# Optimization experiments

Hardware: AMD Instinct MI355X
Metric: run time of the kernel (lower is better)

The kernel has to match this reference:

```python
import jax, jax.numpy as jnp
import numpy as np

B, N, D = 8, 4096, 512

def setup_inputs() -> dict:
    key = jax.random.key(0)
    k1, k2, k3 = jax.random.split(key, 3)
    x = jax.random.normal(k1, (B, N, D), dtype=jnp.float32)
    rotation = jax.random.normal(k2, (D, D), dtype=jnp.float32)
    entangle = jax.random.normal(k3, (D, D), dtype=jnp.float32)
    return {"x": x, "rotation": rotation, "entangle": entangle}

def reference(x, rotation, entangle):
    # query/key projections; note: no V projection, V = x
    query = jnp.einsum("bnd,de->bne", x, rotation)
    key = jnp.einsum("bnd,de->bne", x, entangle)
    scale = 1.0 / jnp.sqrt(jnp.asarray(x.shape[-1], dtype=x.dtype))
    scores = jax.nn.softmax(jnp.einsum("bqd,bkd->bqk", query, key) * scale, axis=-1)
    return jnp.einsum("bqk,bkd->bqd", scores, x)
```

## Files before the change

### kernel.cpp

```cpp
#include <hip/hip_runtime.h>

#define BATCH 8
#define SEQ   4096
#define DIM   512

typedef __attribute__((ext_vector_type(8))) short bf16x8;
typedef __attribute__((ext_vector_type(4))) float f32x4;

__device__ __forceinline__ unsigned short f2bf(float f) {
  unsigned int u = __float_as_uint(f);
  unsigned int r = (u + 0x7fffu + ((u >> 16) & 1u)) >> 16;
  return (unsigned short)r;
}
__device__ __forceinline__ float bf2f(unsigned short s) {
  return __uint_as_float(((unsigned int)s) << 16);
}

__global__ __launch_bounds__(256) void wt_split_kernel(
    const float* __restrict__ rot, const float* __restrict__ ent,
    unsigned short* __restrict__ wrh, unsigned short* __restrict__ wrl,
    unsigned short* __restrict__ weh, unsigned short* __restrict__ wel) {
  const float scale = 0.04419417382415922f;
  int g = blockIdx.x * 256 + threadIdx.x;
  for (int idx = g; idx < 512 * 512; idx += 128 * 256) {
    int d = idx >> 9, e = idx & 511;
    size_t o = (size_t)e * 512 + d;
    float v = rot[idx] * scale;
    unsigned short h = f2bf(v);
    wrh[o] = h; wrl[o] = f2bf(v - bf2f(h));
    float v2 = ent[idx];
    unsigned short h2 = f2bf(v2);
    weh[o] = h2; wel[o] = f2bf(v2 - bf2f(h2));
  }
}

__global__ __launch_bounds__(256) void xt_split_kernel(
    const float* __restrict__ X, unsigned short* __restrict__ Th) {
  __shared__ float T[64][65];
  const int b = blockIdx.z, n0 = blockIdx.x * 64, d0 = blockIdx.y * 64;
  const int tid = threadIdx.x;
  for (int idx = tid; idx < 4096; idx += 256) {
    int r = idx >> 6, c = idx & 63;
    T[r][c] = X[((size_t)(b * SEQ + n0 + r)) * DIM + d0 + c];
  }
  __syncthreads();
  for (int idx = tid; idx < 4096; idx += 256) {
    int r = idx >> 6, c = idx & 63;
    size_t o = ((size_t)(b * DIM + d0 + r)) * SEQ + n0 + c;
    Th[o] = f2bf(T[c][r]);
  }
}

__global__ __launch_bounds__(256, 2) void proj_both(
    const float* __restrict__ X,
    const unsigned short* __restrict__ wrh, const unsigned short* __restrict__ wrl,
    const unsigned short* __restrict__ weh, const unsigned short* __restrict__ wel,
    unsigned short* __restrict__ qh, unsigned short* __restrict__ ql,
    unsigned short* __restrict__ kh, unsigned short* __restrict__ kl) {
  const int tid = threadIdx.x;
  const int w = tid >> 6, lane = tid & 63, l15 = lane & 15, quad = lane >> 4;
  const int rowBase = blockIdx.y * 64 + (w & 1) * 32;
  const int colBase = blockIdx.x * 64 + (w >> 1) * 32;
  f32x4 qa[2][2] = {}, ka[2][2] = {};
  const float* xp[2];
  const unsigned short *rh[2], *rl[2], *eh[2], *el[2];
  xp[0] = X + (size_t)(rowBase + l15) * DIM + quad * 8;
  xp[1] = X + (size_t)(rowBase + 16 + l15) * DIM + quad * 8;
#pragma unroll
  for (int ni = 0; ni < 2; ++ni) {
    size_t o = (size_t)(colBase + ni * 16 + l15) * DIM + quad * 8;
    rh[ni] = wrh + o; rl[ni] = wrl + o; eh[ni] = weh + o; el[ni] = wel + o;
  }
  for (int d0 = 0; d0 < DIM; d0 += 32) {
    bf16x8 ah[2], al[2];
#pragma unroll
    for (int mi = 0; mi < 2; ++mi) {
      const float* p = xp[mi] + d0;
#pragma unroll
      for (int e = 0; e < 8; ++e) {
        float v = p[e];
        unsigned short h = f2bf(v);
        ah[mi][e] = (short)h;
        al[mi][e] = (short)f2bf(v - bf2f(h));
      }
    }
#pragma unroll
    for (int ni = 0; ni < 2; ++ni) {
      bf16x8 bh = *(const bf16x8*)(rh[ni] + d0);
      bf16x8 bl = *(const bf16x8*)(rl[ni] + d0);
      bf16x8 ch = *(const bf16x8*)(eh[ni] + d0);
      bf16x8 cl = *(const bf16x8*)(el[ni] + d0);
#pragma unroll
      for (int mi = 0; mi < 2; ++mi) {
        qa[mi][ni] = __builtin_amdgcn_mfma_f32_16x16x32_bf16(ah[mi], bh, qa[mi][ni], 0, 0, 0);
        qa[mi][ni] = __builtin_amdgcn_mfma_f32_16x16x32_bf16(ah[mi], bl, qa[mi][ni], 0, 0, 0);
        qa[mi][ni] = __builtin_amdgcn_mfma_f32_16x16x32_bf16(al[mi], bh, qa[mi][ni], 0, 0, 0);
        ka[mi][ni] = __builtin_amdgcn_mfma_f32_16x16x32_bf16(ah[mi], ch, ka[mi][ni], 0, 0, 0);
        ka[mi][ni] = __builtin_amdgcn_mfma_f32_16x16x32_bf16(ah[mi], cl, ka[mi][ni], 0, 0, 0);
        ka[mi][ni] = __builtin_amdgcn_mfma_f32_16x16x32_bf16(al[mi], ch, ka[mi][ni], 0, 0, 0);
      }
    }
  }
#pragma unroll
  for (int mi = 0; mi < 2; ++mi)
#pragma unroll
    for (int ni = 0; ni < 2; ++ni)
#pragma unroll
      for (int r = 0; r < 4; ++r) {
        int row = rowBase + mi * 16 + quad * 4 + r;
        int col = colBase + ni * 16 + l15;
        size_t o = (size_t)row * DIM + col;
        float v = qa[mi][ni][r];
        unsigned short h = f2bf(v);
        qh[o] = h; ql[o] = f2bf(v - bf2f(h));
        float v2 = ka[mi][ni][r];
        unsigned short h2 = f2bf(v2);
        kh[o] = h2; kl[o] = f2bf(v2 - bf2f(h2));
      }
}

__global__ __launch_bounds__(256, 2) void attn_mfma(
    const unsigned short* __restrict__ Qh, const unsigned short* __restrict__ Ql,
    const unsigned short* __restrict__ Kh, const unsigned short* __restrict__ Kl,
    const unsigned short* __restrict__ Xth, float* __restrict__ out,
    float* __restrict__ Opart, float* __restrict__ Mp, float* __restrict__ Lp) {
  __shared__ short stage[2][4][2048];
  __shared__ unsigned short PsH[64][72];
  __shared__ float red1[64][2], red2[64][2];
  __shared__ float m_s[64], l_s[64], al_s[64];

  const int tid = threadIdx.x;
  const int w = tid >> 6, lane = tid & 63, l15 = lane & 15, quad = lane >> 4;
  const int b = blockIdx.y, q0 = blockIdx.x * 64;
  const int qsp = (w & 1) * 2, ksp = (w >> 1) * 2;
  const int dbase = w * 128;
  const int ktiles = (SEQ / 64) / gridDim.z;
  const int kbase = blockIdx.z * ktiles * 64;

  if (tid < 64) { m_s[tid] = -3.0e38f; l_s[tid] = 0.0f; }
  __syncthreads();

  f32x4 Of[4][8] = {};

  const int sr = lane >> 2, scm = lane & 3;
  const unsigned short* qsrc = ((w & 1) ? Ql : Qh) + (size_t)(b * SEQ + q0) * DIM;
  const unsigned short* ksrcb = ((w & 1) ? Kl : Kh) + (size_t)b * SEQ * DIM;
  const bool isQ = (w < 2);

  for (int t = 0; t < ktiles; ++t) {
    const int k0 = kbase + t * 64;
    const unsigned short* base = isQ ? qsrc : (ksrcb + (size_t)k0 * DIM);

    {
      bf16x8 g[4];
#pragma unroll
      for (int i = 0; i < 4; ++i) {
        int r = i * 16 + sr, clog = scm ^ (r & 3);
        g[i] = *(const bf16x8*)(base + (size_t)r * DIM + clog * 8);
      }
#pragma unroll
      for (int i = 0; i < 4; ++i) {
        int r = i * 16 + sr;
        *(bf16x8*)&stage[0][w][r * 32 + scm * 8] = g[i];
      }
    }
    __syncthreads();

    f32x4 sa[2][2] = {};
    for (int c = 0; c < 16; ++c) {
      const int bsel = c & 1;
      bf16x8 g[4];
      if (c < 15) {
        const int d0 = (c + 1) * 32;
#pragma unroll
        for (int i = 0; i < 4; ++i) {
          int r = i * 16 + sr, clog = scm ^ (r & 3);
          g[i] = *(const bf16x8*)(base + (size_t)r * DIM + d0 + clog * 8);
        }
      }
      const int cq = (quad ^ (l15 & 3)) * 8;
      bf16x8 a0h = *(const bf16x8*)&stage[bsel][0][((qsp + 0) * 16 + l15) * 32 + cq];
      bf16x8 a0l = *(const bf16x8*)&stage[bsel][1][((qsp + 0) * 16 + l15) * 32 + cq];
      bf16x8 a1h = *(const bf16x8*)&stage[bsel][0][((qsp + 1) * 16 + l15) * 32 + cq];
      bf16x8 a1l = *(const bf16x8*)&stage[bsel][1][((qsp + 1) * 16 + l15) * 32 + cq];
      bf16x8 b0h = *(const bf16x8*)&stage[bsel][2][((ksp + 0) * 16 + l15) * 32 + cq];
      bf16x8 b0l = *(const bf16x8*)&stage[bsel][3][((ksp + 0) * 16 + l15) * 32 + cq];
      bf16x8 b1h = *(const bf16x8*)&stage[bsel][2][((ksp + 1) * 16 + l15) * 32 + cq];
      bf16x8 b1l = *(const bf16x8*)&stage[bsel][3][((ksp + 1) * 16 + l15) * 32 + cq];
      sa[0][0] = __builtin_amdgcn_mfma_f32_16x16x32_bf16(a0h, b0h, sa[0][0], 0, 0, 0);
      sa[0][0] = __builtin_amdgcn_mfma_f32_16x16x32_bf16(a0h, b0l, sa[0][0], 0, 0, 0);
      sa[0][0] = __builtin_amdgcn_mfma_f32_16x16x32_bf16(a0l, b0h, sa[0][0], 0, 0, 0);
      sa[0][1] = __builtin_amdgcn_mfma_f32_16x16x32_bf16(a0h, b1h, sa[0][1], 0, 0, 0);
      sa[0][1] = __builtin_amdgcn_mfma_f32_16x16x32_bf16(a0h, b1l, sa[0][1], 0, 0, 0);
      sa[0][1] = __builtin_amdgcn_mfma_f32_16x16x32_bf16(a0l, b1h, sa[0][1], 0, 0, 0);
      sa[1][0] = __builtin_amdgcn_mfma_f32_16x16x32_bf16(a1h, b0h, sa[1][0], 0, 0, 0);
      sa[1][0] = __builtin_amdgcn_mfma_f32_16x16x32_bf16(a1h, b0l, sa[1][0], 0, 0, 0);
      sa[1][0] = __builtin_amdgcn_mfma_f32_16x16x32_bf16(a1l, b0h, sa[1][0], 0, 0, 0);
      sa[1][1] = __builtin_amdgcn_mfma_f32_16x16x32_bf16(a1h, b1h, sa[1][1], 0, 0, 0);
      sa[1][1] = __builtin_amdgcn_mfma_f32_16x16x32_bf16(a1h, b1l, sa[1][1], 0, 0, 0);
      sa[1][1] = __builtin_amdgcn_mfma_f32_16x16x32_bf16(a1l, b1h, sa[1][1], 0, 0, 0);
      if (c < 15) {
#pragma unroll
        for (int i = 0; i < 4; ++i) {
          int r = i * 16 + sr;
          *(bf16x8*)&stage[1 - bsel][w][r * 32 + scm * 8] = g[i];
        }
      }
      __syncthreads();
    }

    float pm[2][4];
#pragma unroll
    for (int qi = 0; qi < 2; ++qi)
#pragma unroll
      for (int r = 0; r < 4; ++r) {
        float v = fmaxf(sa[qi][0][r], sa[qi][1][r]);
#pragma unroll
        for (int off = 1; off < 16; off <<= 1)
          v = fmaxf(v, __shfl_xor(v, off, 64));
        pm[qi][r] = v;
      }
    if (l15 == 0) {
#pragma unroll
      for (int qi = 0; qi < 2; ++qi)
#pragma unroll
        for (int r = 0; r < 4; ++r)
          red1[(qsp + qi) * 16 + quad * 4 + r][w >> 1] = pm[qi][r];
    }
    __syncthreads();
    if (tid < 64) {
      float mo = m_s[tid];
      float mn = fmaxf(mo, fmaxf(red1[tid][0], red1[tid][1]));
      m_s[tid] = mn;
      al_s[tid] = __expf(mo - mn);
    }
    __syncthreads();

#pragma unroll
    for (int qi = 0; qi < 2; ++qi)
#pragma unroll
      for (int r = 0; r < 4; ++r) {
        const int row = (qsp + qi) * 16 + quad * 4 + r;
        const float m = m_s[row];
        float p0 = __expf(sa[qi][0][r] - m);
        float p1 = __expf(sa[qi][1][r] - m);
        PsH[row][ksp * 16 + l15] = f2bf(p0);
        PsH[row][ksp * 16 + 16 + l15] = f2bf(p1);
        float v = p0 + p1;
#pragma unroll
        for (int off = 1; off < 16; off <<= 1)
          v += __shfl_xor(v, off, 64);
        if (l15 == 0) red2[row][w >> 1] = v;
      }
    __syncthreads();
    if (tid < 64) l_s[tid] = l_s[tid] * al_s[tid] + red2[tid][0] + red2[tid][1];

    float alv[4][4];
#pragma unroll
    for (int qt = 0; qt < 4; ++qt)
#pragma unroll
      for (int r = 0; r < 4; ++r)
        alv[qt][r] = al_s[qt * 16 + quad * 4 + r];
#pragma unroll
    for (int qt = 0; qt < 4; ++qt)
#pragma unroll
      for (int nt = 0; nt < 8; ++nt)
#pragma unroll
        for (int r = 0; r < 4; ++r)
          Of[qt][nt][r] *= alv[qt][r];
#pragma unroll
    for (int ks = 0; ks < 2; ++ks) {
      bf16x8 Ph[4];
#pragma unroll
      for (int qt = 0; qt < 4; ++qt)
        Ph[qt] = *(const bf16x8*)&PsH[qt * 16 + l15][ks * 32 + quad * 8];
      bf16x8 xf[8];
#pragma unroll
      for (int nt = 0; nt < 8; ++nt) {
        const size_t xo =
            ((size_t)(b * DIM + dbase + nt * 16 + l15)) * SEQ + k0 + ks * 32 + quad * 8;
        xf[nt] = *(const bf16x8*)(Xth + xo);
      }
#pragma unroll
      for (int nt = 0; nt < 8; ++nt)
#pragma unroll
        for (int qt = 0; qt < 4; ++qt)
          Of[qt][nt] = __builtin_amdgcn_mfma_f32_16x16x32_bf16(Ph[qt], xf[nt], Of[qt][nt], 0, 0, 0);
    }
    __syncthreads();
  }

  if (gridDim.z == 1) {
    float inv[4][4];
#pragma unroll
    for (int qt = 0; qt < 4; ++qt)
#pragma unroll
      for (int r = 0; r < 4; ++r)
        inv[qt][r] = 1.0f / l_s[qt * 16 + quad * 4 + r];
#pragma unroll
    for (int qt = 0; qt < 4; ++qt)
#pragma unroll
      for (int r = 0; r < 4; ++r) {
        const size_t ro = ((size_t)(b * SEQ + q0 + qt * 16 + quad * 4 + r)) * DIM + dbase;
#pragma unroll
        for (int nt = 0; nt < 8; ++nt)
          out[ro + nt * 16 + l15] = Of[qt][nt][r] * inv[qt][r];
      }
  } else {
    const size_t NE = (size_t)BATCH * SEQ * DIM;
    float* Ob = Opart + (size_t)blockIdx.z * NE;
#pragma unroll
    for (int qt = 0; qt < 4; ++qt)
#pragma unroll
      for (int r = 0; r < 4; ++r) {
        const size_t ro = ((size_t)(b * SEQ + q0 + qt * 16 + quad * 4 + r)) * DIM + dbase;
#pragma unroll
        for (int nt = 0; nt < 8; ++nt)
          Ob[ro + nt * 16 + l15] = Of[qt][nt][r];
      }
    if (tid < 64) {
      size_t ri = (size_t)blockIdx.z * (BATCH * SEQ) + (size_t)b * SEQ + q0 + tid;
      Mp[ri] = m_s[tid];
      Lp[ri] = l_s[tid];
    }
  }
}

__global__ __launch_bounds__(256) void merge_kernel(
    const float* __restrict__ Op, const float* __restrict__ Mp,
    const float* __restrict__ Lp, float* __restrict__ out) {
  const size_t NE = (size_t)BATCH * SEQ * DIM;
  const int NR = BATCH * SEQ;
  size_t i4 = (size_t)blockIdx.x * 256 + threadIdx.x;
  size_t e = i4 * 4;
  int row = (int)(e >> 9);
  float m0 = Mp[row], m1 = Mp[NR + row];
  float l0 = Lp[row], l1 = Lp[NR + row];
  float m = fmaxf(m0, m1);
  float a0 = __expf(m0 - m), a1 = __expf(m1 - m);
  float inv = 1.0f / (a0 * l0 + a1 * l1);
  float4 o0 = *(const float4*)(Op + e);
  float4 o1 = *(const float4*)(Op + NE + e);
  float4 r;
  r.x = (a0 * o0.x + a1 * o1.x) * inv;
  r.y = (a0 * o0.y + a1 * o1.y) * inv;
  r.z = (a0 * o0.z + a1 * o1.z) * inv;
  r.w = (a0 * o0.w + a1 * o1.w) * inv;
  *(float4*)(out + e) = r;
}

extern "C" void kernel_launch(void* const* d_in, const int* in_sizes, int n_in,
                              void* d_out, int out_size, void* d_ws,
                              size_t ws_size, hipStream_t stream) {
  const float* x   = (const float*)d_in[0];
  const float* rot = (const float*)d_in[1];
  const float* ent = (const float*)d_in[2];
  float* out = (float*)d_out;

  const size_t NE = (size_t)BATCH * SEQ * DIM;
  unsigned short* qh  = (unsigned short*)d_ws;
  unsigned short* ql  = qh + NE;
  unsigned short* kh  = ql + NE;
  unsigned short* kl  = kh + NE;
  unsigned short* xth = kl + NE;
  unsigned short* wrh = xth + NE;
  unsigned short* wrl = wrh + 262144;
  unsigned short* weh = wrl + 262144;
  unsigned short* wel = weh + 262144;
  float* Opart = (float*)(wel + 262144);
  float* Mp    = Opart + 2 * NE;
  float* Lp    = Mp + 2 * (BATCH * SEQ);

  const size_t need2 =
      (5 * NE + 4 * 262144) * sizeof(unsigned short) +
      (2 * NE + 4 * (size_t)(BATCH * SEQ)) * sizeof(float);
  const int splits = (ws_size >= need2) ? 2 : 1;

  wt_split_kernel<<<128, 256, 0, stream>>>(rot, ent, wrh, wrl, weh, wel);
  xt_split_kernel<<<dim3(SEQ / 64, DIM / 64, BATCH), 256, 0, stream>>>(x, xth);
  proj_both<<<dim3(DIM / 64, BATCH * SEQ / 64), 256, 0, stream>>>(
      x, wrh, wrl, weh, wel, qh, ql, kh, kl);

  attn_mfma<<<dim3(SEQ / 64, BATCH, splits), 256, 0, stream>>>(
      qh, ql, kh, kl, xth, out, Opart, Mp, Lp);
  if (splits == 2) {
    merge_kernel<<<(unsigned)(NE / 1024), 256, 0, stream>>>(Opart, Mp, Lp, out);
  }
}
```

Baseline: 1.575 ms.

## Restructure attention: register-resident Q, 128-key tiles, direct-to-LDS K loads, presplit X

The attention kernel now keeps each wave's Q fragments (hi/lo bf16) in registers and processes 128 keys per iteration. K tiles stream into LDS through global_load_lds, and the row max and sum are reduced per wave in registers instead of through shared-memory reductions with extra barriers. X is split into bf16 hi/lo once in the transpose kernel, so the projection no longer converts it per tile. Grid ordering is changed, partial output goes straight to out for split 0, and occupancy is raised to 4 blocks. The cost is heavy register pressure (32 Q fragments plus 32 accumulators), which may cause spills at the higher occupancy bound.

```diff
diff --git a/kernel.cpp b/kernel.cpp
--- a/kernel.cpp
+++ b/kernel.cpp
@@ -14,6 +14,12 @@
 }
 __device__ __forceinline__ float bf2f(unsigned short s) {
   return __uint_as_float(((unsigned int)s) << 16);
+}
+
+__device__ __forceinline__ void gload_lds16(const void* g, void* l) {
+  __builtin_amdgcn_global_load_lds(
+      (const __attribute__((address_space(1))) unsigned int*)g,
+      (__attribute__((address_space(3))) unsigned int*)l, 16, 0, 0);
 }
 
 __global__ __launch_bounds__(256) void wt_split_kernel(
@@ -35,13 +41,19 @@
 }
 
 __global__ __launch_bounds__(256) void xt_split_kernel(
-    const float* __restrict__ X, unsigned short* __restrict__ Th) {
+    const float* __restrict__ X, unsigned short* __restrict__ Th,
+    unsigned short* __restrict__ Xh, unsigned short* __restrict__ Xl) {
   __shared__ float T[64][65];
   const int b = blockIdx.z, n0 = blockIdx.x * 64, d0 = blockIdx.y * 64;
   const int tid = threadIdx.x;
   for (int idx = tid; idx < 4096; idx += 256) {
     int r = idx >> 6, c = idx & 63;
-    T[r][c] = X[((size_t)(b * SEQ + n0 + r)) * DIM + d0 + c];
+    size_t gi = ((size_t)(b * SEQ + n0 + r)) * DIM + d0 + c;
+    float v = X[gi];
+    T[r][c] = v;
+    unsigned short h = f2bf(v);
+    Xh[gi] = h;
+    Xl[gi] = f2bf(v - bf2f(h));
   }
   __syncthreads();
   for (int idx = tid; idx < 4096; idx += 256) {
@@ -52,20 +64,23 @@
 }
 
 __global__ __launch_bounds__(256, 2) void proj_both(
-    const float* __restrict__ X,
+    const unsigned short* __restrict__ Xh, const unsigned short* __restrict__ Xl,
     const unsigned short* __restrict__ wrh, const unsigned short* __restrict__ wrl,
     const unsigned short* __restrict__ weh, const unsigned short* __restrict__ wel,
     unsigned short* __restrict__ qh, unsigned short* __restrict__ ql,
     unsigned short* __restrict__ kh, unsigned short* __restrict__ kl) {
   const int tid = threadIdx.x;
   const int w = tid >> 6, lane = tid & 63, l15 = lane & 15, quad = lane >> 4;
-  const int rowBase = blockIdx.y * 64 + (w & 1) * 32;
-  const int colBase = blockIdx.x * 64 + (w >> 1) * 32;
+  const int rowBase = blockIdx.x * 64 + (w & 1) * 32;
+  const int colBase = blockIdx.y * 64 + (w >> 1) * 32;
   f32x4 qa[2][2] = {}, ka[2][2] = {};
-  const float* xp[2];
+  const unsigned short *xph[2], *xpl[2];
   const unsigned short *rh[2], *rl[2], *eh[2], *el[2];
-  xp[0] = X + (size_t)(rowBase + l15) * DIM + quad * 8;
-  xp[1] = X + (size_t)(rowBase + 16 + l15) * DIM + quad * 8;
+#pragma unroll
+  for (int mi = 0; mi < 2; ++mi) {
+    size_t o = (size_t)(rowBase + mi * 16 + l15) * DIM + quad * 8;
+    xph[mi] = Xh + o; xpl[mi] = Xl + o;
+  }
 #pragma unroll
   for (int ni = 0; ni < 2; ++ni) {
     size_t o = (size_t)(colBase + ni * 16 + l15) * DIM + quad * 8;
@@ -75,14 +90,8 @@
     bf16x8 ah[2], al[2];
 #pragma unroll
     for (int mi = 0; mi < 2; ++mi) {
-      const float* p = xp[mi] + d0;
-#pragma unroll
-      for (int e = 0; e < 8; ++e) {
-        float v = p[e];
-        unsigned short h = f2bf(v);
-        ah[mi][e] = (short)h;
-        al[mi][e] = (short)f2bf(v - bf2f(h));
-      }
+      ah[mi] = *(const bf16x8*)(xph[mi] + d0);
+      al[mi] = *(const bf16x8*)(xpl[mi] + d0);
     }
 #pragma unroll
     for (int ni = 0; ni < 2; ++ni) {
@@ -119,161 +128,139 @@
       }
 }
 
-__global__ __launch_bounds__(256, 2) void attn_mfma(
+__global__ __launch_bounds__(256, 4) void attn_mfma(
     const unsigned short* __restrict__ Qh, const unsigned short* __restrict__ Ql,
     const unsigned short* __restrict__ Kh, const unsigned short* __restrict__ Kl,
     const unsigned short* __restrict__ Xth, float* __restrict__ out,
     float* __restrict__ Opart, float* __restrict__ Mp, float* __restrict__ Lp) {
-  __shared__ short stage[2][4][2048];
-  __shared__ unsigned short PsH[64][72];
-  __shared__ float red1[64][2], red2[64][2];
-  __shared__ float m_s[64], l_s[64], al_s[64];
+  __shared__ short stage[2][8192];
+  __shared__ float al_s[64], l_s[64];
+  unsigned short* const PsH = (unsigned short*)&stage[1][0];
 
   const int tid = threadIdx.x;
   const int w = tid >> 6, lane = tid & 63, l15 = lane & 15, quad = lane >> 4;
-  const int b = blockIdx.y, q0 = blockIdx.x * 64;
-  const int qsp = (w & 1) * 2, ksp = (w >> 1) * 2;
+  const int b = blockIdx.x, q0 = blockIdx.y * 64;
+  const int iters = (SEQ / 128) / gridDim.z;
+  const int kbase = blockIdx.z * iters * 128;
   const int dbase = w * 128;
-  const int ktiles = (SEQ / 64) / gridDim.z;
-  const int kbase = blockIdx.z * ktiles * 64;
-
-  if (tid < 64) { m_s[tid] = -3.0e38f; l_s[tid] = 0.0f; }
+
+  bf16x8 qfh[16], qfl[16];
+  {
+    const size_t qrow = (size_t)(b * SEQ + q0 + w * 16 + l15) * DIM + quad * 8;
+#pragma unroll
+    for (int c = 0; c < 16; ++c) {
+      qfh[c] = *(const bf16x8*)(Qh + qrow + c * 32);
+      qfl[c] = *(const bf16x8*)(Ql + qrow + c * 32);
+    }
+  }
+
+  const unsigned short* ksrc[4];
+  int ldsoff[4];
+  {
+#pragma unroll
+    for (int j = 0; j < 4; ++j) {
+      int so = j * 2048 + w * 512 + lane * 8;
+      int plane = so >> 12;
+      int off = so & 4095;
+      int r = off >> 5;
+      int cb = (off >> 3) & 3;
+      int clog = cb ^ (r & 3);
+      ksrc[j] = (plane ? Kl : Kh) + (size_t)(b * SEQ + r) * DIM + clog * 8;
+      ldsoff[j] = j * 2048 + w * 512;
+    }
+  }
+  auto STAGE = [&](int bsel, int krow, int cc) {
+#pragma unroll
+    for (int j = 0; j < 4; ++j)
+      gload_lds16(ksrc[j] + (size_t)krow * DIM + cc * 32,
+                  &stage[bsel][ldsoff[j]]);
+  };
+
+  f32x4 Of[4][8] = {};
+  float m_r[4], l_r[4];
+#pragma unroll
+  for (int r = 0; r < 4; ++r) { m_r[r] = -3.0e38f; l_r[r] = 0.0f; }
+
+  STAGE(0, kbase, 0);
   __syncthreads();
 
-  f32x4 Of[4][8] = {};
-
-  const int sr = lane >> 2, scm = lane & 3;
-  const unsigned short* qsrc = ((w & 1) ? Ql : Qh) + (size_t)(b * SEQ + q0) * DIM;
-  const unsigned short* ksrcb = ((w & 1) ? Kl : Kh) + (size_t)b * SEQ * DIM;
-  const bool isQ = (w < 2);
-
-  for (int t = 0; t < ktiles; ++t) {
-    const int k0 = kbase + t * 64;
-    const unsigned short* base = isQ ? qsrc : (ksrcb + (size_t)k0 * DIM);
-
-    {
-      bf16x8 g[4];
-#pragma unroll
-      for (int i = 0; i < 4; ++i) {
-        int r = i * 16 + sr, clog = scm ^ (r & 3);
-        g[i] = *(const bf16x8*)(base + (size_t)r * DIM + clog * 8);
-      }
-#pragma unroll
-      for (int i = 0; i < 4; ++i) {
-        int r = i * 16 + sr;
-        *(bf16x8*)&stage[0][w][r * 32 + scm * 8] = g[i];
-      }
+  for (int t = 0; t < iters; ++t) {
+    const int k0 = kbase + t * 128;
+    f32x4 sa[8] = {};
+
+#pragma unroll
+    for (int c = 0; c < 16; ++c) {
+      if (c < 15) STAGE((c + 1) & 1, k0, c + 1);
+      const short* bufp = &stage[c & 1][0];
+      const int cq = (quad ^ (l15 & 3)) * 8;
+#pragma unroll
+      for (int s = 0; s < 8; ++s) {
+        const int kr = s * 16 + l15;
+        bf16x8 bh = *(const bf16x8*)(bufp + kr * 32 + cq);
+        bf16x8 bl = *(const bf16x8*)(bufp + 4096 + kr * 32 + cq);
+        sa[s] = __builtin_amdgcn_mfma_f32_16x16x32_bf16(qfh[c], bh, sa[s], 0, 0, 0);
+        sa[s] = __builtin_amdgcn_mfma_f32_16x16x32_bf16(qfh[c], bl, sa[s], 0, 0, 0);
+        sa[s] = __builtin_amdgcn_mfma_f32_16x16x32_bf16(qfl[c], bh, sa[s], 0, 0, 0);
+      }
+      __syncthreads();
+    }
+
+    float al_r[4];
+#pragma unroll
+    for (int r = 0; r < 4; ++r) {
+      float v = sa[0][r];
+#pragma unroll
+      for (int s = 1; s < 8; ++s) v = fmaxf(v, sa[s][r]);
+#pragma unroll
+      for (int off = 1; off < 16; off <<= 1) v = fmaxf(v, __shfl_xor(v, off, 64));
+      float mn = fmaxf(m_r[r], v);
+      al_r[r] = __expf(m_r[r] - mn);
+      m_r[r] = mn;
+    }
+#pragma unroll
+    for (int r = 0; r < 4; ++r) {
+      const int row = w * 16 + quad * 4 + r, rx = row & 15;
+      float sum = 0.0f;
+#pragma unroll
+      for (int s = 0; s < 8; ++s) {
+        float p = __expf(sa[s][r] - m_r[r]);
+        sum += p;
+        const int col = s * 16 + l15;
+        PsH[row * 128 + ((col >> 3) ^ rx) * 8 + (col & 7)] = f2bf(p);
+      }
+#pragma unroll
+      for (int off = 1; off < 16; off <<= 1) sum += __shfl_xor(sum, off, 64);
+      l_r[r] = l_r[r] * al_r[r] + sum;
+    }
+    if (l15 == 0) {
+#pragma unroll
+      for (int r = 0; r < 4; ++r) al_s[w * 16 + quad * 4 + r] = al_r[r];
     }
     __syncthreads();
 
-    f32x4 sa[2][2] = {};
-    for (int c = 0; c < 16; ++c) {
-      const int bsel = c & 1;
-      bf16x8 g[4];
-      if (c < 15) {
-        const int d0 = (c + 1) * 32;
-#pragma unroll
-        for (int i = 0; i < 4; ++i) {
-          int r = i * 16 + sr, clog = scm ^ (r & 3);
-          g[i] = *(const bf16x8*)(base + (size_t)r * DIM + d0 + clog * 8);
-        }
-      }
-      const int cq = (quad ^ (l15 & 3)) * 8;
-      bf16x8 a0h = *(const bf16x8*)&stage[bsel][0][((qsp + 0) * 16 + l15) * 32 + cq];
-      bf16x8 a0l = *(const bf16x8*)&stage[bsel][1][((qsp + 0) * 16 + l15) * 32 + cq];
-      bf16x8 a1h = *(const bf16x8*)&stage[bsel][0][((qsp + 1) * 16 + l15) * 32 + cq];
-      bf16x8 a1l = *(const bf16x8*)&stage[bsel][1][((qsp + 1) * 16 + l15) * 32 + cq];
-      bf16x8 b0h = *(const bf16x8*)&stage[bsel][2][((ksp + 0) * 16 + l15) * 32 + cq];
-      bf16x8 b0l = *(const bf16x8*)&stage[bsel][3][((ksp + 0) * 16 + l15) * 32 + cq];
-      bf16x8 b1h = *(const bf16x8*)&stage[bsel][2][((ksp + 1) * 16 + l15) * 32 + cq];
-      bf16x8 b1l = *(const bf16x8*)&stage[bsel][3][((ksp + 1) * 16 + l15) * 32 + cq];
-      sa[0][0] = __builtin_amdgcn_mfma_f32_16x16x32_bf16(a0h, b0h, sa[0][0], 0, 0, 0);
-      sa[0][0] = __builtin_amdgcn_mfma_f32_16x16x32_bf16(a0h, b0l, sa[0][0], 0, 0, 0);
-      sa[0][0] = __builtin_amdgcn_mfma_f32_16x16x32_bf16(a0l, b0h, sa[0][0], 0, 0, 0);
-      sa[0][1] = __builtin_amdgcn_mfma_f32_16x16x32_bf16(a0h, b1h, sa[0][1], 0, 0, 0);
-      sa[0][1] = __builtin_amdgcn_mfma_f32_16x16x32_bf16(a0h, b1l, sa[0][1], 0, 0, 0);
-      sa[0][1] = __builtin_amdgcn_mfma_f32_16x16x32_bf16(a0l, b1h, sa[0][1], 0, 0, 0);
-      sa[1][0] = __builtin_amdgcn_mfma_f32_16x16x32_bf16(a1h, b0h, sa[1][0], 0, 0, 0);
-      sa[1][0] = __builtin_amdgcn_mfma_f32_16x16x32_bf16(a1h, b0l, sa[1][0], 0, 0, 0);
-      sa[1][0] = __builtin_amdgcn_mfma_f32_16x16x32_bf16(a1l, b0h, sa[1][0], 0, 0, 0);
-      sa[1][1] = __builtin_amdgcn_mfma_f32_16x16x32_bf16(a1h, b1h, sa[1][1], 0, 0, 0);
-      sa[1][1] = __builtin_amdgcn_mfma_f32_16x16x32_bf16(a1h, b1l, sa[1][1], 0, 0, 0);
-      sa[1][1] = __builtin_amdgcn_mfma_f32_16x16x32_bf16(a1l, b1h, sa[1][1], 0, 0, 0);
-      if (c < 15) {
-#pragma unroll
-        for (int i = 0; i < 4; ++i) {
-          int r = i * 16 + sr;
-          *(bf16x8*)&stage[1 - bsel][w][r * 32 + scm * 8] = g[i];
-        }
-      }
-      __syncthreads();
-    }
-
-    float pm[2][4];
-#pragma unroll
-    for (int qi = 0; qi < 2; ++qi)
-#pragma unroll
-      for (int r = 0; r < 4; ++r) {
-        float v = fmaxf(sa[qi][0][r], sa[qi][1][r]);
-#pragma unroll
-        for (int off = 1; off < 16; off <<= 1)
-          v = fmaxf(v, __shfl_xor(v, off, 64));
-        pm[qi][r] = v;
-      }
-    if (l15 == 0) {
-#pragma unroll
-      for (int qi = 0; qi < 2; ++qi)
-#pragma unroll
-        for (int r = 0; r < 4; ++r)
-          red1[(qsp + qi) * 16 + quad * 4 + r][w >> 1] = pm[qi][r];
-    }
-    __syncthreads();
-    if (tid < 64) {
-      float mo = m_s[tid];
-      float mn = fmaxf(mo, fmaxf(red1[tid][0], red1[tid][1]));
-      m_s[tid] = mn;
-      al_s[tid] = __expf(mo - mn);
-    }
-    __syncthreads();
-
-#pragma unroll
-    for (int qi = 0; qi < 2; ++qi)
-#pragma unroll
-      for (int r = 0; r < 4; ++r) {
-        const int row = (qsp + qi) * 16 + quad * 4 + r;
-        const float m = m_s[row];
-        float p0 = __expf(sa[qi][0][r] - m);
-        float p1 = __expf(sa[qi][1][r] - m);
-        PsH[row][ksp * 16 + l15] = f2bf(p0);
-        PsH[row][ksp * 16 + 16 + l15] = f2bf(p1);
-        float v = p0 + p1;
-#pragma unroll
-        for (int off = 1; off < 16; off <<= 1)
-          v += __shfl_xor(v, off, 64);
-        if (l15 == 0) red2[row][w >> 1] = v;
-      }
-    __syncthreads();
-    if (tid < 64) l_s[tid] = l_s[tid] * al_s[tid] + red2[tid][0] + red2[tid][1];
-
     float alv[4][4];
 #pragma unroll
     for (int qt = 0; qt < 4; ++qt)
 #pragma unroll
-      for (int r = 0; r < 4; ++r)
-        alv[qt][r] = al_s[qt * 16 + quad * 4 + r];
+      for (int r = 0; r < 4; ++r) alv[qt][r] = al_s[qt * 16 + quad * 4 + r];
 #pragma unroll
     for (int qt = 0; qt < 4; ++qt)
 #pragma unroll
       for (int nt = 0; nt < 8; ++nt)
 #pragma unroll
-        for (int r = 0; r < 4; ++r)
-          Of[qt][nt][r] *= alv[qt][r];
-#pragma unroll
-    for (int ks = 0; ks < 2; ++ks) {
+        for (int r = 0; r < 4; ++r) Of[qt][nt][r] *= alv[qt][r];
+
+    if (t + 1 < iters) STAGE(0, k0 + 128, 0);
+
+#pragma unroll
+    for (int ks = 0; ks < 4; ++ks) {
       bf16x8 Ph[4];
 #pragma unroll
-      for (int qt = 0; qt < 4; ++qt)
-        Ph[qt] = *(const bf16x8*)&PsH[qt * 16 + l15][ks * 32 + quad * 8];
+      for (int qt = 0; qt < 4; ++qt) {
+        const int prow = qt * 16 + l15;
+        const int sb = (ks * 4 + quad) ^ l15;
+        Ph[qt] = *(const bf16x8*)(PsH + prow * 128 + sb * 8);
+      }
       bf16x8 xf[8];
 #pragma unroll
       for (int nt = 0; nt < 8; ++nt) {
@@ -290,57 +277,57 @@
     __syncthreads();
   }
 
+  if (l15 == 0) {
+#pragma unroll
+    for (int r = 0; r < 4; ++r) l_s[w * 16 + quad * 4 + r] = l_r[r];
+    if (gridDim.z > 1) {
+      size_t ri = (size_t)blockIdx.z * (BATCH * SEQ) + (size_t)b * SEQ + q0 + w * 16 + quad * 4;
+#pragma unroll
+      for (int r = 0; r < 4; ++r) { Mp[ri + r] = m_r[r]; Lp[ri + r] = l_r[r]; }
+    }
+  }
+  __syncthreads();
+
   if (gridDim.z == 1) {
     float inv[4][4];
 #pragma unroll
     for (int qt = 0; qt < 4; ++qt)
 #pragma unroll
-      for (int r = 0; r < 4; ++r)
-        inv[qt][r] = 1.0f / l_s[qt * 16 + quad * 4 + r];
+      for (int r = 0; r < 4; ++r) inv[qt][r] = 1.0f / l_s[qt * 16 + quad * 4 + r];
 #pragma unroll
     for (int qt = 0; qt < 4; ++qt)
 #pragma unroll
       for (int r = 0; r < 4; ++r) {
         const size_t ro = ((size_t)(b * SEQ + q0 + qt * 16 + quad * 4 + r)) * DIM + dbase;
 #pragma unroll
-        for (int nt = 0; nt < 8; ++nt)
-          out[ro + nt * 16 + l15] = Of[qt][nt][r] * inv[qt][r];
+        for (int nt = 0; nt < 8; ++nt) out[ro + nt * 16 + l15] = Of[qt][nt][r] * inv[qt][r];
       }
   } else {
-    const size_t NE = (size_t)BATCH * SEQ * DIM;
-    float* Ob = Opart + (size_t)blockIdx.z * NE;
+    float* Ob = (blockIdx.z == 0) ? out : Opart;
 #pragma unroll
     for (int qt = 0; qt < 4; ++qt)
 #pragma unroll
       for (int r = 0; r < 4; ++r) {
         const size_t ro = ((size_t)(b * SEQ + q0 + qt * 16 + quad * 4 + r)) * DIM + dbase;
 #pragma unroll
-        for (int nt = 0; nt < 8; ++nt)
-          Ob[ro + nt * 16 + l15] = Of[qt][nt][r];
-      }
-    if (tid < 64) {
-      size_t ri = (size_t)blockIdx.z * (BATCH * SEQ) + (size_t)b * SEQ + q0 + tid;
-      Mp[ri] = m_s[tid];
-      Lp[ri] = l_s[tid];
-    }
+        for (int nt = 0; nt < 8; ++nt) Ob[ro + nt * 16 + l15] = Of[qt][nt][r];
+      }
   }
 }
 
 __global__ __launch_bounds__(256) void merge_kernel(
-    const float* __restrict__ Op, const float* __restrict__ Mp,
-    const float* __restrict__ Lp, float* __restrict__ out) {
-  const size_t NE = (size_t)BATCH * SEQ * DIM;
+    float* __restrict__ out, const float* __restrict__ Op,
+    const float* __restrict__ Mp, const float* __restrict__ Lp) {
   const int NR = BATCH * SEQ;
-  size_t i4 = (size_t)blockIdx.x * 256 + threadIdx.x;
-  size_t e = i4 * 4;
+  size_t e = ((size_t)blockIdx.x * 256 + threadIdx.x) * 4;
   int row = (int)(e >> 9);
   float m0 = Mp[row], m1 = Mp[NR + row];
   float l0 = Lp[row], l1 = Lp[NR + row];
   float m = fmaxf(m0, m1);
   float a0 = __expf(m0 - m), a1 = __expf(m1 - m);
   float inv = 1.0f / (a0 * l0 + a1 * l1);
-  float4 o0 = *(const float4*)(Op + e);
-  float4 o1 = *(const float4*)(Op + NE + e);
+  float4 o0 = *(const float4*)(out + e);
+  float4 o1 = *(const float4*)(Op + e);
   float4 r;
   r.x = (a0 * o0.x + a1 * o1.x) * inv;
   r.y = (a0 * o0.y + a1 * o1.y) * inv;
@@ -363,27 +350,29 @@
   unsigned short* kh  = ql + NE;
   unsigned short* kl  = kh + NE;
   unsigned short* xth = kl + NE;
-  unsigned short* wrh = xth + NE;
+  unsigned short* xh  = xth + NE;
+  unsigned short* xl  = xh + NE;
+  unsigned short* wrh = xl + NE;
   unsigned short* wrl = wrh + 262144;
   unsigned short* weh = wrl + 262144;
   unsigned short* wel = weh + 262144;
   float* Opart = (float*)(wel + 262144);
-  float* Mp    = Opart + 2 * NE;
+  float* Mp    = Opart + NE;
   float* Lp    = Mp + 2 * (BATCH * SEQ);
 
   const size_t need2 =
-      (5 * NE + 4 * 262144) * sizeof(unsigned short) +
-      (2 * NE + 4 * (size_t)(BATCH * SEQ)) * sizeof(float);
+      (7 * NE + 4 * 262144) * sizeof(unsigned short) +
+      (NE + 4 * (size_t)(BATCH * SEQ)) * sizeof(float);
   const int splits = (ws_size >= need2) ? 2 : 1;
 
   wt_split_kernel<<<128, 256, 0, stream>>>(rot, ent, wrh, wrl, weh, wel);
-  xt_split_kernel<<<dim3(SEQ / 64, DIM / 64, BATCH), 256, 0, stream>>>(x, xth);
-  proj_both<<<dim3(DIM / 64, BATCH * SEQ / 64), 256, 0, stream>>>(
-      x, wrh, wrl, weh, wel, qh, ql, kh, kl);
-
-  attn_mfma<<<dim3(SEQ / 64, BATCH, splits), 256, 0, stream>>>(
+  xt_split_kernel<<<dim3(SEQ / 64, DIM / 64, BATCH), 256, 0, stream>>>(x, xth, xh, xl);
+  proj_both<<<dim3(BATCH * SEQ / 64, DIM / 64), 256, 0, stream>>>(
+      xh, xl, wrh, wrl, weh, wel, qh, ql, kh, kl);
+
+  attn_mfma<<<dim3(BATCH, SEQ / 64, splits), 256, 0, stream>>>(
       qh, ql, kh, kl, xth, out, Opart, Mp, Lp);
   if (splits == 2) {
-    merge_kernel<<<(unsigned)(NE / 1024), 256, 0, stream>>>(Opart, Mp, Lp, out);
-  }
-}
+    merge_kernel<<<(unsigned)(NE / 1024), 256, 0, stream>>>(out, Opart, Mp, Lp);
+  }
+}
```

Result: slower. 4.058 ms (+157.7%).
